# Optimization experiments

Measured on AMD Instinct MI355X. Metric: run time of the kernel, lower is better.

The kernel has to match this reference:

```python
import jax, jax.numpy as jnp
import numpy as np

B_, T_, D_MODEL = 2, 2048, 1024
EXPAND, D_STATE, D_CONV, HEADDIM = 2, 128, 4, 64
D_INNER = EXPAND * D_MODEL            # 2048
NHEADS = D_INNER // HEADDIM           # 32
CONV_DIM = D_INNER + 2 * D_STATE      # 2304 (x, B, C share the depthwise conv)
D_IN_PROJ = 2 * D_INNER + 2 * D_STATE + NHEADS  # z, xBC, dt


def _rmsnorm(x, w, eps=1e-5):
    return x * jax.lax.rsqrt(jnp.mean(x * x, axis=-1, keepdims=True) + eps) * w


def setup_inputs() -> dict:
    key = jax.random.key(0)
    ks = jax.random.split(key, 8)
    def s(k, shape, scale=0.02):
        return jax.random.normal(k, shape, jnp.float32) * scale
    x = jax.random.normal(ks[0], (B_, T_, D_MODEL), jnp.float32)
    W_in = s(ks[1], (D_MODEL, D_IN_PROJ))
    conv_w = s(ks[2], (CONV_DIM, D_CONV), 0.1)
    conv_b = jnp.zeros((CONV_DIM,), jnp.float32)
    # dt_bias = softplus^-1(dt_init) with dt in [1e-3, 1e-1], per Mamba init
    dt0 = jax.random.uniform(ks[3], (NHEADS,), minval=1e-3, maxval=1e-1)
    dt_bias = jnp.log(jnp.expm1(dt0))
    A_log = jnp.log(jax.random.uniform(ks[4], (NHEADS,), minval=1.0, maxval=16.0))
    D = jnp.ones((NHEADS,), jnp.float32)
    norm_w = jnp.ones((D_MODEL,), jnp.float32)
    gnorm_w = jnp.ones((D_INNER,), jnp.float32)
    W_out = s(ks[5], (D_INNER, D_MODEL))
    return {"x": x, "W_in": W_in, "conv_w": conv_w, "conv_b": conv_b,
            "dt_bias": dt_bias, "A_log": A_log, "D": D,
            "norm_w": norm_w, "gnorm_w": gnorm_w, "W_out": W_out}


def reference(x, W_in, conv_w, conv_b, dt_bias, A_log, D, norm_w, gnorm_w, W_out):
    res = x
    xn = _rmsnorm(x, norm_w)                       # pre-norm
    zxbcdt = xn @ W_in                             # (B,T,D_IN_PROJ)
    z = zxbcdt[..., :D_INNER]
    xBC = zxbcdt[..., D_INNER:D_INNER + CONV_DIM]
    dt = zxbcdt[..., D_INNER + CONV_DIM:]          # (B,T,H)
    # causal depthwise conv over time on concat(x,B,C)
    inp = jnp.transpose(xBC, (0, 2, 1))            # (B,C,T)
    kern = conv_w[:, None, :]                      # (C,1,K)
    conv = jax.lax.conv_general_dilated(
        inp, kern, window_strides=(1,), padding=[(D_CONV - 1, 0)],
        feature_group_count=CONV_DIM, dimension_numbers=("NCH", "OIH", "NCH"))
    xBC = jax.nn.silu(jnp.transpose(conv, (0, 2, 1)) + conv_b)
    xs = xBC[..., :D_INNER].reshape(B_, T_, NHEADS, HEADDIM)  # (B,T,H,P)
    Bm = xBC[..., D_INNER:D_INNER + D_STATE]       # (B,T,N), ngroups=1
    C = xBC[..., D_INNER + D_STATE:]               # (B,T,N)
    dt = jax.nn.softplus(dt + dt_bias)             # (B,T,H)
    A = -jnp.exp(A_log)                            # (H,)

    def step(h, inps):
        x_t, B_t, C_t, dt_t = inps                 # (B,H,P),(B,N),(B,N),(B,H)
        da = jnp.exp(dt_t * A)                     # (B,H)
        h = h * da[:, :, None, None] + (dt_t[..., None] * x_t)[..., None] * B_t[:, None, None, :]
        y = jnp.einsum("bhpn,bn->bhp", h, C_t) + D[None, :, None] * x_t
        return h, y

    h0 = jnp.zeros((B_, NHEADS, HEADDIM, D_STATE), x.dtype)
    seq = (jnp.moveaxis(xs, 1, 0), jnp.moveaxis(Bm, 1, 0),
           jnp.moveaxis(C, 1, 0), jnp.moveaxis(dt, 1, 0))
    _, ys = jax.lax.scan(step, h0, seq)            # ys: (T,B,H,P)
    y = jnp.moveaxis(ys, 0, 1).reshape(B_, T_, D_INNER)
    y = _rmsnorm(y * jax.nn.silu(z), gnorm_w)      # gated RMSNorm
    return y @ W_out + res
```

## Files before the change

kernel.cpp:

```cpp
#include <hip/hip_runtime.h>
#include <hip/hip_bf16.h>

typedef unsigned short u16;
typedef unsigned int u32;
typedef u16 u16x8 __attribute__((ext_vector_type(8)));
typedef __bf16 bf16x8 __attribute__((ext_vector_type(8)));
typedef float f32x4 __attribute__((ext_vector_type(4)));

#define B_SZ 2
#define T_SZ 2048
#define DMODEL 1024
#define DINNER 2048
#define DSTATE 128
#define NHEADS 32
#define HEADDIM 64
#define CONVDIM 2304
#define DINPROJ 4384
#define DINPROJ_P 4480
#define NROWS (B_SZ * T_SZ)
#define L_CH 128
#define NCH 16

__device__ __forceinline__ float bf2f(u16 u) {
    union { float f; u32 i; } v; v.i = ((u32)u) << 16; return v.f;
}
__device__ __forceinline__ u16 f2bf(float f) {
    union { float f; u32 i; } v; v.f = f;
    u32 r = v.i + 0x7FFFu + ((v.i >> 16) & 1u);
    return (u16)(r >> 16);
}
__device__ __forceinline__ bf16x8 ldfrag(const u16* p) {
    return __builtin_bit_cast(bf16x8, *(const u16x8*)p);
}
__device__ __forceinline__ void gload_lds16(const u16* g, u16* l) {
    __builtin_amdgcn_global_load_lds(
        (const __attribute__((address_space(1))) unsigned int*)g,
        (__attribute__((address_space(3))) unsigned int*)l, 16, 0, 0);
}

__device__ void trans_tile(const float* __restrict__ in, u16* __restrict__ out,
                           int K, int N, int n0, int k0)
{
    __shared__ u16 tile[64][66];
    const int tid = threadIdx.x;
#pragma unroll
    for (int r = 0; r < 16; r++) {
        int idx = r * 256 + tid;
        int k = idx >> 6, n = idx & 63;
        float v = (n0 + n < N) ? in[(size_t)(k0 + k) * N + n0 + n] : 0.f;
        tile[n][k] = f2bf(v);
    }
    __syncthreads();
#pragma unroll
    for (int r = 0; r < 16; r++) {
        int idx = r * 256 + tid;
        int n = idx >> 6, k = idx & 63;
        out[(size_t)(n0 + n) * K + k0 + k] = tile[n][k];
    }
}

__global__ __launch_bounds__(256) void prep_kernel(
    const float* __restrict__ W_in, u16* __restrict__ W_inT,
    const float* __restrict__ W_out, u16* __restrict__ W_outT,
    const float* __restrict__ x, const float* __restrict__ nw, u16* __restrict__ xn,
    const float* __restrict__ cw, u16* __restrict__ cwT)
{
    const int blk = blockIdx.x;
    const int tid = threadIdx.x;
    if (blk < 1120) {
        trans_tile(W_in, W_inT, DMODEL, DINPROJ, (blk % 70) * 64, (blk / 70) * 64);
    } else if (blk < 1632) {
        int idx = blk - 1120;
        trans_tile(W_out, W_outT, DINNER, DMODEL, (idx % 16) * 64, (idx / 16) * 64);
    } else if (blk < 5728) {
        const int row = blk - 1632;
        const float* xr = x + (size_t)row * DMODEL;
        float vals[4]; float ss = 0.f;
#pragma unroll
        for (int i = 0; i < 4; i++) {
            int c = tid + i * 256;
            float v = xr[c]; vals[i] = v; ss += v * v;
        }
#pragma unroll
        for (int o = 32; o; o >>= 1) ss += __shfl_xor(ss, o);
        __shared__ float red[4];
        if ((tid & 63) == 0) red[tid >> 6] = ss;
        __syncthreads();
        ss = red[0] + red[1] + red[2] + red[3];
        float sc = rsqrtf(ss / (float)DMODEL + 1e-5f);
#pragma unroll
        for (int i = 0; i < 4; i++) {
            int c = tid + i * 256;
            xn[(size_t)row * DMODEL + c] = f2bf(vals[i] * sc * nw[c]);
        }
    } else {
        for (int idx = tid; idx < 4 * CONVDIM; idx += 256) {
            int k = idx / CONVDIM, c = idx - k * CONVDIM;
            cwT[idx] = f2bf(cw[c * 4 + k]);
        }
    }
}

template<int MODE, int KC>
__global__ __launch_bounds__(256) void gemm128_kernel(
    const u16* __restrict__ A, const u16* __restrict__ BT, void* __restrict__ Cv,
    const float* __restrict__ Res, int Nst, int nbx)
{
    __shared__ u16 As[128 * 64];
    __shared__ u16 Bs[128 * 64];
    const int tid = threadIdx.x;
    const int l = tid & 63, w = tid >> 6;
    const int per = nbx * 8;
    const int grp = blockIdx.x / per, r = blockIdx.x % per;
    const int m0 = (grp * 8 + (r & 7)) * 128;
    const int n0 = (r >> 3) * 128;
    const int ml = l & 15, quad = l >> 4;
    const int wm = (w & 1) * 64, wn = (w >> 1) * 64;
    f32x4 acc[4][4] = {};
    const int srow = l >> 3;
    const int sgx = (l & 7) ^ srow;
    const u16* Ag = A + (size_t)(m0 + w * 8 + srow) * KC + sgx * 8;
    const u16* Bg = BT + (size_t)(n0 + w * 8 + srow) * KC + sgx * 8;
    u16* const As_w = &As[(w * 8) * 64];
    u16* const Bs_w = &Bs[(w * 8) * 64];

#pragma unroll 4
    for (int k0 = 0; k0 < KC; k0 += 64) {
        __syncthreads();
#pragma unroll
        for (int j = 0; j < 4; j++) {
            gload_lds16(Ag + (size_t)(j * 32) * KC + k0, As_w + j * 32 * 64);
            gload_lds16(Bg + (size_t)(j * 32) * KC + k0, Bs_w + j * 32 * 64);
        }
        __syncthreads();
#pragma unroll
        for (int ks4 = 0; ks4 < 2; ks4++) {
            bf16x8 af[4], bfr[4];
#pragma unroll
            for (int i = 0; i < 4; i++)
                af[i] = ldfrag(&As[(wm + i * 16 + ml) * 64 +
                                   (((ks4 * 4 + quad) ^ (ml & 7)) * 8)]);
#pragma unroll
            for (int i = 0; i < 4; i++)
                bfr[i] = ldfrag(&Bs[(wn + i * 16 + ml) * 64 +
                                    (((ks4 * 4 + quad) ^ (ml & 7)) * 8)]);
#pragma unroll
            for (int mt = 0; mt < 4; mt++)
#pragma unroll
                for (int nt = 0; nt < 4; nt++)
                    acc[mt][nt] = __builtin_amdgcn_mfma_f32_16x16x32_bf16(
                        af[mt], bfr[nt], acc[mt][nt], 0, 0, 0);
        }
    }
#pragma unroll
    for (int mt = 0; mt < 4; mt++)
#pragma unroll
        for (int nt = 0; nt < 4; nt++)
#pragma unroll
            for (int rg = 0; rg < 4; rg++) {
                int m = m0 + wm + mt * 16 + quad * 4 + rg;
                int n = n0 + wn + nt * 16 + ml;
                if (n < Nst) {
                    if (MODE == 0)
                        ((u16*)Cv)[(size_t)m * Nst + n] = f2bf(acc[mt][nt][rg]);
                    else
                        ((float*)Cv)[(size_t)m * Nst + n] =
                            acc[mt][nt][rg] + Res[(size_t)m * Nst + n];
                }
            }
}

template<int KC>
__global__ __launch_bounds__(256) void gemm128x64_kernel(
    const u16* __restrict__ A, const u16* __restrict__ BT, float* __restrict__ C,
    const float* __restrict__ Res, int Nst)
{
    __shared__ u16 As[128 * 64];
    __shared__ u16 Bs[64 * 64];
    const int tid = threadIdx.x;
    const int l = tid & 63, w = tid >> 6;
    const int m0 = blockIdx.y * 128;
    const int n0 = blockIdx.x * 64;
    const int ml = l & 15, quad = l >> 4;
    const int wm = w * 32;
    f32x4 acc[2][4] = {};
    const int srow = l >> 3;
    const int sgx = (l & 7) ^ srow;
    const u16* Ag = A + (size_t)(m0 + w * 8 + srow) * KC + sgx * 8;
    const u16* Bg = BT + (size_t)(n0 + w * 8 + srow) * KC + sgx * 8;
    u16* const As_w = &As[(w * 8) * 64];
    u16* const Bs_w = &Bs[(w * 8) * 64];

#pragma unroll 4
    for (int k0 = 0; k0 < KC; k0 += 64) {
        __syncthreads();
#pragma unroll
        for (int j = 0; j < 4; j++)
            gload_lds16(Ag + (size_t)(j * 32) * KC + k0, As_w + j * 32 * 64);
#pragma unroll
        for (int j = 0; j < 2; j++)
            gload_lds16(Bg + (size_t)(j * 32) * KC + k0, Bs_w + j * 32 * 64);
        __syncthreads();
#pragma unroll
        for (int ks4 = 0; ks4 < 2; ks4++) {
            bf16x8 af[2], bfr[4];
#pragma unroll
            for (int i = 0; i < 2; i++)
                af[i] = ldfrag(&As[(wm + i * 16 + ml) * 64 +
                                   (((ks4 * 4 + quad) ^ (ml & 7)) * 8)]);
#pragma unroll
            for (int i = 0; i < 4; i++)
                bfr[i] = ldfrag(&Bs[(i * 16 + ml) * 64 +
                                    (((ks4 * 4 + quad) ^ (ml & 7)) * 8)]);
#pragma unroll
            for (int mt = 0; mt < 2; mt++)
#pragma unroll
                for (int nt = 0; nt < 4; nt++)
                    acc[mt][nt] = __builtin_amdgcn_mfma_f32_16x16x32_bf16(
                        af[mt], bfr[nt], acc[mt][nt], 0, 0, 0);
        }
    }
#pragma unroll
    for (int mt = 0; mt < 2; mt++)
#pragma unroll
        for (int nt = 0; nt < 4; nt++)
#pragma unroll
            for (int rg = 0; rg < 4; rg++) {
                int m = m0 + wm + mt * 16 + quad * 4 + rg;
                int n = n0 + nt * 16 + ml;
                C[(size_t)m * Nst + n] = acc[mt][nt][rg] + Res[(size_t)m * Nst + n];
            }
}

#define NGRAN (CONVDIM / 8)
__global__ __launch_bounds__(256) void conv_silu_kernel(
    const u16* __restrict__ zx, const u16* __restrict__ cwT,
    const float* __restrict__ cb, const float* __restrict__ dt_bias,
    u16* __restrict__ out, float* __restrict__ dts)
{
    int idx = blockIdx.x * 256 + threadIdx.x;
    if (idx < B_SZ * NHEADS * T_SZ) {
        int t = idx & (T_SZ - 1);
        int bh = idx >> 11;
        int h = bh & 31, b = bh >> 5;
        float v = bf2f(zx[(size_t)(b * T_SZ + t) * DINPROJ + (DINNER + CONVDIM) + h]) + dt_bias[h];
        float sp = (v > 20.f) ? v : log1pf(expf(v));
        dts[((size_t)bh << 11) + t] = sp;
    }
    int gr = idx % NGRAN;
    int bt = idx / NGRAN;
    int t = bt & (T_SZ - 1);
    int c0 = gr * 8;
    float acc[8];
#pragma unroll
    for (int u = 0; u < 8; u++) acc[u] = cb[c0 + u];
    const u16* base = zx + (size_t)bt * DINPROJ + DINNER + c0;
#pragma unroll
    for (int k = 0; k < 4; k++) {
        int tt = t - 3 + k;
        if (tt >= 0) {
            u16x8 xv = *(const u16x8*)(base + (ptrdiff_t)(k - 3) * DINPROJ);
            u16x8 wv = *(const u16x8*)&cwT[k * CONVDIM + c0];
#pragma unroll
            for (int u = 0; u < 8; u++)
                acc[u] += bf2f(xv[u]) * bf2f(wv[u]);
        }
    }
    u16 res[8];
#pragma unroll
    for (int u = 0; u < 8; u++) {
        float s = acc[u] / (1.f + expf(-acc[u]));
        res[u] = f2bf(s);
    }
    *(u16x8*)&out[(size_t)bt * CONVDIM + c0] = *(u16x8*)res;
}

__global__ __launch_bounds__(256) void chunk_state_kernel(
    const u16* __restrict__ xbc, const float* __restrict__ dts_g,
    const float* __restrict__ A_log, float* __restrict__ cs_g, u16* __restrict__ S_bf)
{
    const int g = blockIdx.x;
    const int b = g >> 9, rem = g & 511, c = rem >> 5, h = rem & 31;
    const int tid = threadIdx.x;
    __shared__ float tmp[128], dt_l[128], d2e[128];
    __shared__ u16 Xw[64][136];
    __shared__ u16 BsT[128][136];
    const float A = -__expf(A_log[h]);
    if (tid < 128) {
        float d = dts_g[(((size_t)(b * 32 + h)) << 11) + (c << 7) + tid];
        dt_l[tid] = d; tmp[tid] = d * A;
    }
    __syncthreads();
    for (int off = 1; off < 128; off <<= 1) {
        float add = 0.f;
        if (tid < 128 && tid >= off) add = tmp[tid - off];
        __syncthreads();
        if (tid < 128) tmp[tid] += add;
        __syncthreads();
    }
    if (tid < 128) {
        float cs = tmp[tid];
        cs_g[(((size_t)(b * 32 + h)) << 11) + (c << 7) + tid] = cs;
        d2e[tid] = __expf(tmp[127] - cs) * dt_l[tid];
    }
    __syncthreads();
    const size_t rowbase = ((size_t)(b * T_SZ + c * L_CH)) * CONVDIM;
#pragma unroll
    for (int r = 0; r < 4; r++) {
        int v = tid + r * 256;
        int t = v >> 3, p0 = (v & 7) << 3;
        u16x8 xv = *(const u16x8*)&xbc[rowbase + (size_t)t * CONVDIM + h * 64 + p0];
        float s = d2e[t];
#pragma unroll
        for (int u = 0; u < 8; u++) Xw[p0 + u][t] = f2bf(bf2f(xv[u]) * s);
    }
#pragma unroll
    for (int r = 0; r < 8; r++) {
        int v = tid + r * 256;
        int t = v >> 4, n0 = (v & 15) << 3;
        u16x8 bv = *(const u16x8*)&xbc[rowbase + (size_t)t * CONVDIM + DINNER + n0];
#pragma unroll
        for (int u = 0; u < 8; u++) BsT[n0 + u][t] = bv[u];
    }
    __syncthreads();
    const int lane = tid & 63, wv = tid >> 6, ml = lane & 15, quad = lane >> 4;
    f32x4 acc[8] = {};
    for (int k0 = 0; k0 < 128; k0 += 32) {
        bf16x8 af = ldfrag(&Xw[wv * 16 + ml][k0 + quad * 8]);
#pragma unroll
        for (int nt = 0; nt < 8; nt++) {
            bf16x8 bf = ldfrag(&BsT[nt * 16 + ml][k0 + quad * 8]);
            acc[nt] = __builtin_amdgcn_mfma_f32_16x16x32_bf16(af, bf, acc[nt], 0, 0, 0);
        }
    }
    const size_t base = (size_t)g * 8192;
#pragma unroll
    for (int nt = 0; nt < 8; nt++) {
#pragma unroll
        for (int rg = 0; rg < 4; rg++) {
            int p = wv * 16 + quad * 4 + rg, n = nt * 16 + ml;
            S_bf[base + p * 128 + n] = f2bf(acc[nt][rg]);
        }
    }
}

__global__ __launch_bounds__(256) void state_pass_kernel(
    const float* __restrict__ cs_g, u16* __restrict__ S_bf)
{
    const int bh = blockIdx.x, b = bh >> 5, h = bh & 31;
    const int tid = threadIdx.x;
    float H[32];
#pragma unroll
    for (int i = 0; i < 32; i++) H[i] = 0.f;
    for (int c = 0; c < NCH; c++) {
        float decay = __expf(cs_g[(((size_t)(b * 32 + h)) << 11) + (c << 7) + 127]);
        size_t slot = ((size_t)((b * NCH + c) * 32 + h)) * 8192 + tid * 32;
        u16 tv[32];
#pragma unroll
        for (int q = 0; q < 4; q++)
            *(u16x8*)&tv[q * 8] = *(const u16x8*)&S_bf[slot + q * 8];
        u16 hw[32];
#pragma unroll
        for (int i = 0; i < 32; i++) hw[i] = f2bf(H[i]);
#pragma unroll
        for (int q = 0; q < 4; q++)
            *(u16x8*)&S_bf[slot + q * 8] = *(const u16x8*)&hw[q * 8];
#pragma unroll
        for (int i = 0; i < 32; i++) H[i] = H[i] * decay + bf2f(tv[i]);
    }
}

__global__ __launch_bounds__(256) void chunk_out_kernel(
    const u16* __restrict__ xbc, const float* __restrict__ dts_g,
    const float* __restrict__ cs_g, const u16* __restrict__ H_bf,
    const float* __restrict__ Dv, u16* __restrict__ yraw)
{
    const int g = blockIdx.x;
    const int b = g >> 9, rem = g & 511, c = rem >> 5, h = rem & 31;
    const int tid = threadIdx.x;
    __shared__ u16 Xs[64][136];
    __shared__ u16 Gs[128][40];
    __shared__ float cs_l[128], P_l[128], dt_l[128];
    const size_t rowbase = ((size_t)(b * T_SZ + c * L_CH)) * CONVDIM;
    const u16* Cg = xbc + rowbase + DINNER + 128;
    const u16* Bg = xbc + rowbase + DINNER;
    const u16* Hg = H_bf + (size_t)g * 8192;
    if (tid < 128) {
        float cs = cs_g[(((size_t)(b * 32 + h)) << 11) + (c << 7) + tid];
        cs_l[tid] = cs; P_l[tid] = __expf(cs);
        dt_l[tid] = dts_g[(((size_t)(b * 32 + h)) << 11) + (c << 7) + tid];
    }
#pragma unroll
    for (int r = 0; r < 4; r++) {
        int v = tid + r * 256; int t = v >> 3, p0 = (v & 7) << 3;
        u16x8 xv = *(const u16x8*)&xbc[rowbase + (size_t)t * CONVDIM + h * 64 + p0];
#pragma unroll
        for (int u = 0; u < 8; u++) Xs[p0 + u][t] = xv[u];
    }
    __syncthreads();
    const int lane = tid & 63, wv = tid >> 6, ml = lane & 15, quad = lane >> 4;
    const int trow = wv * 32;
    f32x4 accY[2][4] = {};
    for (int k0 = 0; k0 < 128; k0 += 32) {
        bf16x8 af0 = ldfrag(Cg + (size_t)(trow + ml) * CONVDIM + k0 + quad * 8);
        bf16x8 af1 = ldfrag(Cg + (size_t)(trow + 16 + ml) * CONVDIM + k0 + quad * 8);
#pragma unroll
        for (int pt = 0; pt < 4; pt++) {
            bf16x8 bf = ldfrag(Hg + (pt * 16 + ml) * 128 + k0 + quad * 8);
            accY[0][pt] = __builtin_amdgcn_mfma_f32_16x16x32_bf16(af0, bf, accY[0][pt], 0, 0, 0);
            accY[1][pt] = __builtin_amdgcn_mfma_f32_16x16x32_bf16(af1, bf, accY[1][pt], 0, 0, 0);
        }
    }
#pragma unroll
    for (int mt = 0; mt < 2; mt++) {
#pragma unroll
        for (int rg = 0; rg < 4; rg++) {
            float pp = P_l[trow + mt * 16 + quad * 4 + rg];
#pragma unroll
            for (int pt = 0; pt < 4; pt++) accY[mt][pt][rg] *= pp;
        }
    }
    for (int js = 0; js < 4; js++) {
        const int j0 = js * 32;
        f32x4 Ga[2][2] = {};
        for (int k0 = 0; k0 < 128; k0 += 32) {
            bf16x8 af0 = ldfrag(Cg + (size_t)(trow + ml) * CONVDIM + k0 + quad * 8);
            bf16x8 af1 = ldfrag(Cg + (size_t)(trow + 16 + ml) * CONVDIM + k0 + quad * 8);
            bf16x8 bf0 = ldfrag(Bg + (size_t)(j0 + ml) * CONVDIM + k0 + quad * 8);
            bf16x8 bf1 = ldfrag(Bg + (size_t)(j0 + 16 + ml) * CONVDIM + k0 + quad * 8);
            Ga[0][0] = __builtin_amdgcn_mfma_f32_16x16x32_bf16(af0, bf0, Ga[0][0], 0, 0, 0);
            Ga[0][1] = __builtin_amdgcn_mfma_f32_16x16x32_bf16(af0, bf1, Ga[0][1], 0, 0, 0);
            Ga[1][0] = __builtin_amdgcn_mfma_f32_16x16x32_bf16(af1, bf0, Ga[1][0], 0, 0, 0);
            Ga[1][1] = __builtin_amdgcn_mfma_f32_16x16x32_bf16(af1, bf1, Ga[1][1], 0, 0, 0);
        }
#pragma unroll
        for (int mt = 0; mt < 2; mt++) {
#pragma unroll
            for (int jt = 0; jt < 2; jt++) {
#pragma unroll
                for (int rg = 0; rg < 4; rg++) {
                    int t = trow + mt * 16 + quad * 4 + rg;
                    int j = j0 + jt * 16 + ml;
                    float val = 0.f;
                    if (t >= j) val = Ga[mt][jt][rg] * __expf(cs_l[t] - cs_l[j]) * dt_l[j];
                    Gs[t][jt * 16 + ml] = f2bf(val);
                }
            }
        }
#pragma unroll
        for (int mt = 0; mt < 2; mt++) {
            bf16x8 af = ldfrag(&Gs[trow + mt * 16 + ml][quad * 8]);
#pragma unroll
            for (int pt = 0; pt < 4; pt++) {
                bf16x8 bf = ldfrag(&Xs[pt * 16 + ml][j0 + quad * 8]);
                accY[mt][pt] = __builtin_amdgcn_mfma_f32_16x16x32_bf16(af, bf, accY[mt][pt], 0, 0, 0);
            }
        }
    }
    const float Dh = Dv[h];
    const size_t ybase = ((size_t)(b * T_SZ + c * L_CH)) * DINNER;
#pragma unroll
    for (int mt = 0; mt < 2; mt++) {
#pragma unroll
        for (int pt = 0; pt < 4; pt++) {
#pragma unroll
            for (int rg = 0; rg < 4; rg++) {
                int t = trow + mt * 16 + quad * 4 + rg;
                int p = pt * 16 + ml;
                float v = accY[mt][pt][rg] + Dh * bf2f(Xs[p][t]);
                yraw[ybase + (size_t)t * DINNER + h * 64 + p] = f2bf(v);
            }
        }
    }
}

__global__ __launch_bounds__(256) void postnorm_kernel(
    const u16* __restrict__ yraw, const u16* __restrict__ zx,
    const float* __restrict__ gw, u16* __restrict__ out)
{
    const int row = blockIdx.x;
    const u16* yr = yraw + (size_t)row * DINNER;
    const u16* zr = zx + (size_t)row * DINPROJ;
    float vals[8]; float ss = 0.f;
#pragma unroll
    for (int i = 0; i < 8; i++) {
        int c = threadIdx.x + i * 256;
        float y = bf2f(yr[c]);
        float z = bf2f(zr[c]);
        float s = z / (1.f + expf(-z));
        float t = y * s; vals[i] = t; ss += t * t;
    }
#pragma unroll
    for (int o = 32; o; o >>= 1) ss += __shfl_xor(ss, o);
    __shared__ float red[4];
    if ((threadIdx.x & 63) == 0) red[threadIdx.x >> 6] = ss;
    __syncthreads();
    ss = red[0] + red[1] + red[2] + red[3];
    float sc = rsqrtf(ss / (float)DINNER + 1e-5f);
#pragma unroll
    for (int i = 0; i < 8; i++) {
        int c = threadIdx.x + i * 256;
        out[(size_t)row * DINNER + c] = f2bf(vals[i] * sc * gw[c]);
    }
}

extern "C" void kernel_launch(void* const* d_in, const int* in_sizes, int n_in,
                              void* d_out, int out_size, void* d_ws, size_t ws_size,
                              hipStream_t stream) {
    const float* x       = (const float*)d_in[0];
    const float* W_in    = (const float*)d_in[1];
    const float* conv_w  = (const float*)d_in[2];
    const float* conv_b  = (const float*)d_in[3];
    const float* dt_bias = (const float*)d_in[4];
    const float* A_log   = (const float*)d_in[5];
    const float* Dv      = (const float*)d_in[6];
    const float* norm_w  = (const float*)d_in[7];
    const float* gnorm_w = (const float*)d_in[8];
    const float* W_out   = (const float*)d_in[9];
    float* out = (float*)d_out;

    char* ws = (char*)d_ws;
    u16*   xn    = (u16*)(ws);
    u16*   W_inT = (u16*)(ws + 8388608);
    u16*   S_bf  = (u16*)(ws);
    float* cs_g  = (float*)(ws + 16777216);
    u16*   zx    = (u16*)(ws + 17563648);
    u16*   xbc   = (u16*)(ws + 53477376);
    float* dts   = (float*)(ws + 72351744);
    u16*   yraw  = (u16*)(ws + 72876032);
    u16*   cwT   = (u16*)(ws + 89653248);
    u16*   W_outT= (u16*)(ws + 89671680);
    u16*   ynorm = yraw;

    prep_kernel<<<5729, 256, 0, stream>>>(
        W_in, W_inT, W_out, W_outT, x, norm_w, xn, conv_w, cwT);
    gemm128_kernel<0, DMODEL><<<(DINPROJ_P / 128) * (NROWS / 128), 256, 0, stream>>>(
        xn, W_inT, zx, nullptr, DINPROJ, DINPROJ_P / 128);
    conv_silu_kernel<<<(NROWS * NGRAN) / 256, 256, 0, stream>>>(
        zx, cwT, conv_b, dt_bias, xbc, dts);
    chunk_state_kernel<<<B_SZ * NCH * NHEADS, 256, 0, stream>>>(xbc, dts, A_log, cs_g, S_bf);
    state_pass_kernel<<<B_SZ * NHEADS, 256, 0, stream>>>(cs_g, S_bf);
    chunk_out_kernel<<<B_SZ * NCH * NHEADS, 256, 0, stream>>>(xbc, dts, cs_g, S_bf, Dv, yraw);
    postnorm_kernel<<<NROWS, 256, 0, stream>>>(yraw, zx, gnorm_w, ynorm);
    gemm128x64_kernel<DINNER><<<dim3(DMODEL / 64, NROWS / 128), 256, 0, stream>>>(
        ynorm, W_outT, out, x, DMODEL);
}
```

Measured before the change: 299.1 us.

## Pipeline in-projection GEMM with 256x256 tiles and vectorize memory-bound kernels

Replaces the 128x128 in-projection GEMM with a 512-thread 256x256-tile kernel. It double-buffers LDS, interleaves global-to-LDS staging with MFMA sub-steps, and raises wave priority during the matrix ops. The leftover columns are handled by a separate 128x64 GEMM launch. It also vectorizes the weight transpose, RMSNorm prep and postnorm loads/stores, and spreads the state-pass across 8x more blocks with 4 elements per thread. The larger tile trades a smaller grid (256 blocks) and heavier register/LDS use for better data reuse.

```diff
diff --git a/kernel.cpp b/kernel.cpp
--- a/kernel.cpp
+++ b/kernel.cpp
@@ -4,6 +4,7 @@
 typedef unsigned short u16;
 typedef unsigned int u32;
 typedef u16 u16x8 __attribute__((ext_vector_type(8)));
+typedef u16 u16x4 __attribute__((ext_vector_type(4)));
 typedef __bf16 bf16x8 __attribute__((ext_vector_type(8)));
 typedef float f32x4 __attribute__((ext_vector_type(4)));
 
@@ -41,21 +42,34 @@
 __device__ void trans_tile(const float* __restrict__ in, u16* __restrict__ out,
                            int K, int N, int n0, int k0)
 {
-    __shared__ u16 tile[64][66];
+    __shared__ u16 tile[64][72];
     const int tid = threadIdx.x;
 #pragma unroll
-    for (int r = 0; r < 16; r++) {
+    for (int r = 0; r < 4; r++) {
         int idx = r * 256 + tid;
-        int k = idx >> 6, n = idx & 63;
-        float v = (n0 + n < N) ? in[(size_t)(k0 + k) * N + n0 + n] : 0.f;
-        tile[n][k] = f2bf(v);
+        int k = idx >> 4, n4 = (idx & 15) << 2;
+        const float* src = &in[(size_t)(k0 + k) * N + n0 + n4];
+        float4 v;
+        if (n0 + n4 + 3 < N) {
+            v = *(const float4*)src;
+        } else {
+            v.x = (n0 + n4 + 0 < N) ? src[0] : 0.f;
+            v.y = (n0 + n4 + 1 < N) ? src[1] : 0.f;
+            v.z = (n0 + n4 + 2 < N) ? src[2] : 0.f;
+            v.w = (n0 + n4 + 3 < N) ? src[3] : 0.f;
+        }
+        tile[n4 + 0][k] = f2bf(v.x);
+        tile[n4 + 1][k] = f2bf(v.y);
+        tile[n4 + 2][k] = f2bf(v.z);
+        tile[n4 + 3][k] = f2bf(v.w);
     }
     __syncthreads();
 #pragma unroll
-    for (int r = 0; r < 16; r++) {
+    for (int r = 0; r < 2; r++) {
         int idx = r * 256 + tid;
-        int n = idx >> 6, k = idx & 63;
-        out[(size_t)(n0 + n) * K + k0 + k] = tile[n][k];
+        int n = idx >> 3, k8 = (idx & 7) << 3;
+        u16x8 vv = *(const u16x8*)&tile[n][k8];
+        *(u16x8*)&out[(size_t)(n0 + n) * K + k0 + k8] = vv;
     }
 }
 
@@ -74,13 +88,8 @@
         trans_tile(W_out, W_outT, DINNER, DMODEL, (idx % 16) * 64, (idx / 16) * 64);
     } else if (blk < 5728) {
         const int row = blk - 1632;
-        const float* xr = x + (size_t)row * DMODEL;
-        float vals[4]; float ss = 0.f;
-#pragma unroll
-        for (int i = 0; i < 4; i++) {
-            int c = tid + i * 256;
-            float v = xr[c]; vals[i] = v; ss += v * v;
-        }
+        float4 v = ((const float4*)(x + (size_t)row * DMODEL))[tid];
+        float ss = v.x * v.x + v.y * v.y + v.z * v.z + v.w * v.w;
 #pragma unroll
         for (int o = 32; o; o >>= 1) ss += __shfl_xor(ss, o);
         __shared__ float red[4];
@@ -88,11 +97,13 @@
         __syncthreads();
         ss = red[0] + red[1] + red[2] + red[3];
         float sc = rsqrtf(ss / (float)DMODEL + 1e-5f);
-#pragma unroll
-        for (int i = 0; i < 4; i++) {
-            int c = tid + i * 256;
-            xn[(size_t)row * DMODEL + c] = f2bf(vals[i] * sc * nw[c]);
-        }
+        float4 wv = ((const float4*)nw)[tid];
+        u16x4 o4;
+        o4[0] = f2bf(v.x * sc * wv.x);
+        o4[1] = f2bf(v.y * sc * wv.y);
+        o4[2] = f2bf(v.z * sc * wv.z);
+        o4[3] = f2bf(v.w * sc * wv.w);
+        *(u16x4*)&xn[(size_t)row * DMODEL + tid * 4] = o4;
     } else {
         for (int idx = tid; idx < 4 * CONVDIM; idx += 256) {
             int k = idx / CONVDIM, c = idx - k * CONVDIM;
@@ -101,79 +112,122 @@
     }
 }
 
-template<int MODE, int KC>
-__global__ __launch_bounds__(256) void gemm128_kernel(
-    const u16* __restrict__ A, const u16* __restrict__ BT, void* __restrict__ Cv,
-    const float* __restrict__ Res, int Nst, int nbx)
-{
-    __shared__ u16 As[128 * 64];
-    __shared__ u16 Bs[128 * 64];
+template<int KC>
+__global__ __launch_bounds__(512, 2) void gemm256_kernel(
+    const u16* __restrict__ A, const u16* __restrict__ BT, u16* __restrict__ C,
+    int Nst, int Brows, int nbn)
+{
+    __shared__ u16 As[2 * 256 * 64];
+    __shared__ u16 Bs[2 * 256 * 64];
     const int tid = threadIdx.x;
     const int l = tid & 63, w = tid >> 6;
-    const int per = nbx * 8;
-    const int grp = blockIdx.x / per, r = blockIdx.x % per;
-    const int m0 = (grp * 8 + (r & 7)) * 128;
-    const int n0 = (r >> 3) * 128;
+    const int wm = w >> 2, wn = w & 3;
     const int ml = l & 15, quad = l >> 4;
-    const int wm = (w & 1) * 64, wn = (w >> 1) * 64;
-    f32x4 acc[4][4] = {};
-    const int srow = l >> 3;
-    const int sgx = (l & 7) ^ srow;
-    const u16* Ag = A + (size_t)(m0 + w * 8 + srow) * KC + sgx * 8;
-    const u16* Bg = BT + (size_t)(n0 + w * 8 + srow) * KC + sgx * 8;
-    u16* const As_w = &As[(w * 8) * 64];
-    u16* const Bs_w = &Bs[(w * 8) * 64];
-
-#pragma unroll 4
-    for (int k0 = 0; k0 < KC; k0 += 64) {
-        __syncthreads();
-#pragma unroll
-        for (int j = 0; j < 4; j++) {
-            gload_lds16(Ag + (size_t)(j * 32) * KC + k0, As_w + j * 32 * 64);
-            gload_lds16(Bg + (size_t)(j * 32) * KC + k0, Bs_w + j * 32 * 64);
-        }
-        __syncthreads();
-#pragma unroll
-        for (int ks4 = 0; ks4 < 2; ks4++) {
-            bf16x8 af[4], bfr[4];
-#pragma unroll
-            for (int i = 0; i < 4; i++)
-                af[i] = ldfrag(&As[(wm + i * 16 + ml) * 64 +
-                                   (((ks4 * 4 + quad) ^ (ml & 7)) * 8)]);
-#pragma unroll
-            for (int i = 0; i < 4; i++)
-                bfr[i] = ldfrag(&Bs[(wn + i * 16 + ml) * 64 +
-                                    (((ks4 * 4 + quad) ^ (ml & 7)) * 8)]);
-#pragma unroll
-            for (int mt = 0; mt < 4; mt++)
-#pragma unroll
-                for (int nt = 0; nt < 4; nt++)
-                    acc[mt][nt] = __builtin_amdgcn_mfma_f32_16x16x32_bf16(
-                        af[mt], bfr[nt], acc[mt][nt], 0, 0, 0);
-        }
-    }
-#pragma unroll
-    for (int mt = 0; mt < 4; mt++)
+    const int srow = l >> 3, sgx = (l & 7) ^ srow;
+
+    const int bid = blockIdx.x;
+    const int wg = (bid & 7) * (gridDim.x >> 3) + (bid >> 3);
+    const int m0 = (wg / nbn) * 256;
+    const int n0 = (wg % nbn) * 256;
+    const int bcap = Brows - 1 - n0;
+
+    const u16* Ag = A + (size_t)m0 * KC;
+    const u16* Bg = BT + (size_t)n0 * KC;
+    const int NT = KC / 64;
+
+    f32x4 acc[8][4] = {};
+    bf16x8 af[4][2];
+    bf16x8 bfr[2][2][2];
+
+#define BARX() { asm volatile("" ::: "memory"); __builtin_amdgcn_s_barrier(); asm volatile("" ::: "memory"); }
+#define STG(Gp, Lp, bsel, hs, kt, cap)                                        \
+    { const int kcol_ = (kt) * 64;                                            \
+      _Pragma("unroll")                                                       \
+      for (int j_ = 0; j_ < 2; j_++) {                                        \
+          const int i0_ = (w * 2 + j_) * 8;                                   \
+          const int r0_ = (i0_ & 63) + ((i0_ >> 6) << 7) + ((hs) << 6);       \
+          int gr_ = r0_ + srow; if (gr_ > (cap)) gr_ = (cap);                 \
+          gload_lds16(Gp + (size_t)gr_ * KC + kcol_ + sgx * 8,                \
+                      Lp + (bsel) * 16384 + r0_ * 64);                        \
+      } }
+#define RDA(bsel, qm)                                                         \
+    _Pragma("unroll") for (int mt_ = 0; mt_ < 4; mt_++)                       \
+    _Pragma("unroll") for (int ks_ = 0; ks_ < 2; ks_++)                       \
+        af[mt_][ks_] = ldfrag(&As[(bsel) * 16384 +                            \
+            (wm * 128 + ((qm) * 4 + mt_) * 16 + ml) * 64 +                    \
+            (((ks_ * 4 + quad) ^ (ml & 7)) * 8)]);
+#define RDB(bsel, qn)                                                         \
+    _Pragma("unroll") for (int nt_ = 0; nt_ < 2; nt_++)                       \
+    _Pragma("unroll") for (int ks_ = 0; ks_ < 2; ks_++)                       \
+        bfr[qn][nt_][ks_] = ldfrag(&Bs[(bsel) * 16384 +                       \
+            (wn * 64 + ((qn) * 2 + nt_) * 16 + ml) * 64 +                     \
+            (((ks_ * 4 + quad) ^ (ml & 7)) * 8)]);
+#define MMA(qm, qn)                                                           \
+    __builtin_amdgcn_s_setprio(1);                                            \
+    _Pragma("unroll") for (int ks_ = 0; ks_ < 2; ks_++)                       \
+    _Pragma("unroll") for (int mt_ = 0; mt_ < 4; mt_++)                       \
+    _Pragma("unroll") for (int nt_ = 0; nt_ < 2; nt_++)                       \
+        acc[(qm) * 4 + mt_][(qn) * 2 + nt_] =                                 \
+            __builtin_amdgcn_mfma_f32_16x16x32_bf16(                          \
+                af[mt_][ks_], bfr[qn][nt_][ks_],                              \
+                acc[(qm) * 4 + mt_][(qn) * 2 + nt_], 0, 0, 0);                \
+    __builtin_amdgcn_s_setprio(0);
+
+    STG(Ag, As, 0, 0, 0, 255);
+    STG(Bg, Bs, 0, 0, 0, bcap);
+    STG(Bg, Bs, 0, 1, 0, bcap);
+    STG(Ag, As, 0, 1, 0, bcap < 255 ? bcap : 255);
+    STG(Ag, As, 1, 0, 1, 255);
+    STG(Bg, Bs, 1, 0, 1, bcap);
+    asm volatile("s_waitcnt vmcnt(4)" ::: "memory");
+    BARX();
+
+#define TILE(t, bsel)                                                         \
+    { const bool s1_ = (t) + 1 < NT, s2_ = (t) + 2 < NT;                      \
+      RDA(bsel, 0); RDB(bsel, 0);                                             \
+      if (s1_) STG(Bg, Bs, (bsel) ^ 1, 1, (t) + 1, bcap);                     \
+      BARX(); MMA(0, 0); BARX();                                              \
+      RDB(bsel, 1);                                                           \
+      if (s1_) STG(Ag, As, (bsel) ^ 1, 1, (t) + 1, 255);                      \
+      BARX(); MMA(0, 1); BARX();                                              \
+      RDA(bsel, 1);                                                           \
+      if (s2_) STG(Ag, As, bsel, 0, (t) + 2, 255);                            \
+      BARX(); MMA(1, 0); BARX();                                              \
+      if (s2_) { STG(Bg, Bs, bsel, 0, (t) + 2, bcap);                         \
+                 asm volatile("s_waitcnt vmcnt(4)" ::: "memory"); }           \
+      else     { asm volatile("s_waitcnt vmcnt(0)" ::: "memory"); }           \
+      BARX(); MMA(1, 1); BARX(); }
+
+#pragma unroll 1
+    for (int t = 0; t < NT; t += 2) {
+        TILE(t, 0);
+        TILE(t + 1, 1);
+    }
+#undef TILE
+#undef MMA
+#undef RDB
+#undef RDA
+#undef STG
+#undef BARX
+
+#pragma unroll
+    for (int mt = 0; mt < 8; mt++)
 #pragma unroll
         for (int nt = 0; nt < 4; nt++)
 #pragma unroll
             for (int rg = 0; rg < 4; rg++) {
-                int m = m0 + wm + mt * 16 + quad * 4 + rg;
-                int n = n0 + wn + nt * 16 + ml;
-                if (n < Nst) {
-                    if (MODE == 0)
-                        ((u16*)Cv)[(size_t)m * Nst + n] = f2bf(acc[mt][nt][rg]);
-                    else
-                        ((float*)Cv)[(size_t)m * Nst + n] =
-                            acc[mt][nt][rg] + Res[(size_t)m * Nst + n];
-                }
+                int m = m0 + wm * 128 + mt * 16 + quad * 4 + rg;
+                int n = n0 + wn * 64 + nt * 16 + ml;
+                if (n < Nst)
+                    C[(size_t)m * Nst + n] = f2bf(acc[mt][nt][rg]);
             }
 }
 
-template<int KC>
+
+template<int KC, int MODE>
 __global__ __launch_bounds__(256) void gemm128x64_kernel(
-    const u16* __restrict__ A, const u16* __restrict__ BT, float* __restrict__ C,
-    const float* __restrict__ Res, int Nst)
+    const u16* __restrict__ A, const u16* __restrict__ BT, void* __restrict__ Cv,
+    const float* __restrict__ Res, int Nst, int Nlim)
 {
     __shared__ u16 As[128 * 64];
     __shared__ u16 Bs[64 * 64];
@@ -228,7 +282,13 @@
             for (int rg = 0; rg < 4; rg++) {
                 int m = m0 + wm + mt * 16 + quad * 4 + rg;
                 int n = n0 + nt * 16 + ml;
-                C[(size_t)m * Nst + n] = acc[mt][nt][rg] + Res[(size_t)m * Nst + n];
+                if (n < Nlim) {
+                    if (MODE == 0)
+                        ((u16*)Cv)[(size_t)m * Nst + n] = f2bf(acc[mt][nt][rg]);
+                    else
+                        ((float*)Cv)[(size_t)m * Nst + n] =
+                            acc[mt][nt][rg] + Res[(size_t)m * Nst + n];
+                }
             }
 }
 
@@ -347,26 +407,20 @@
 __global__ __launch_bounds__(256) void state_pass_kernel(
     const float* __restrict__ cs_g, u16* __restrict__ S_bf)
 {
-    const int bh = blockIdx.x, b = bh >> 5, h = bh & 31;
-    const int tid = threadIdx.x;
-    float H[32];
-#pragma unroll
-    for (int i = 0; i < 32; i++) H[i] = 0.f;
+    const int bh = blockIdx.x >> 3, b = bh >> 5, h = bh & 31;
+    const int off = (blockIdx.x & 7) * 1024 + threadIdx.x * 4;
+    const float* csb = cs_g + (((size_t)(b * 32 + h)) << 11);
+    float H[4] = {0.f, 0.f, 0.f, 0.f};
     for (int c = 0; c < NCH; c++) {
-        float decay = __expf(cs_g[(((size_t)(b * 32 + h)) << 11) + (c << 7) + 127]);
-        size_t slot = ((size_t)((b * NCH + c) * 32 + h)) * 8192 + tid * 32;
-        u16 tv[32];
-#pragma unroll
-        for (int q = 0; q < 4; q++)
-            *(u16x8*)&tv[q * 8] = *(const u16x8*)&S_bf[slot + q * 8];
-        u16 hw[32];
-#pragma unroll
-        for (int i = 0; i < 32; i++) hw[i] = f2bf(H[i]);
-#pragma unroll
-        for (int q = 0; q < 4; q++)
-            *(u16x8*)&S_bf[slot + q * 8] = *(const u16x8*)&hw[q * 8];
-#pragma unroll
-        for (int i = 0; i < 32; i++) H[i] = H[i] * decay + bf2f(tv[i]);
+        float decay = __expf(csb[(c << 7) + 127]);
+        size_t slot = ((size_t)((b * NCH + c) * 32 + h)) * 8192 + off;
+        u16x4 tv = *(const u16x4*)&S_bf[slot];
+        u16x4 hw;
+#pragma unroll
+        for (int i = 0; i < 4; i++) hw[i] = f2bf(H[i]);
+        *(u16x4*)&S_bf[slot] = hw;
+#pragma unroll
+        for (int i = 0; i < 4; i++) H[i] = H[i] * decay + bf2f(tv[i]);
     }
 }
 
@@ -479,29 +533,28 @@
     const float* __restrict__ gw, u16* __restrict__ out)
 {
     const int row = blockIdx.x;
-    const u16* yr = yraw + (size_t)row * DINNER;
-    const u16* zr = zx + (size_t)row * DINPROJ;
+    const int tid = threadIdx.x;
+    u16x8 yv = *(const u16x8*)(yraw + (size_t)row * DINNER + tid * 8);
+    u16x8 zv = *(const u16x8*)(zx + (size_t)row * DINPROJ + tid * 8);
     float vals[8]; float ss = 0.f;
 #pragma unroll
     for (int i = 0; i < 8; i++) {
-        int c = threadIdx.x + i * 256;
-        float y = bf2f(yr[c]);
-        float z = bf2f(zr[c]);
+        float y = bf2f(yv[i]);
+        float z = bf2f(zv[i]);
         float s = z / (1.f + expf(-z));
         float t = y * s; vals[i] = t; ss += t * t;
     }
 #pragma unroll
     for (int o = 32; o; o >>= 1) ss += __shfl_xor(ss, o);
     __shared__ float red[4];
-    if ((threadIdx.x & 63) == 0) red[threadIdx.x >> 6] = ss;
+    if ((tid & 63) == 0) red[tid >> 6] = ss;
     __syncthreads();
     ss = red[0] + red[1] + red[2] + red[3];
     float sc = rsqrtf(ss / (float)DINNER + 1e-5f);
-#pragma unroll
-    for (int i = 0; i < 8; i++) {
-        int c = threadIdx.x + i * 256;
-        out[(size_t)row * DINNER + c] = f2bf(vals[i] * sc * gw[c]);
-    }
+    u16 o8[8];
+#pragma unroll
+    for (int i = 0; i < 8; i++) o8[i] = f2bf(vals[i] * sc * gw[tid * 8 + i]);
+    *(u16x8*)(out + (size_t)row * DINNER + tid * 8) = *(u16x8*)o8;
 }
 
 extern "C" void kernel_launch(void* const* d_in, const int* in_sizes, int n_in,
@@ -534,14 +587,17 @@
 
     prep_kernel<<<5729, 256, 0, stream>>>(
         W_in, W_inT, W_out, W_outT, x, norm_w, xn, conv_w, cwT);
-    gemm128_kernel<0, DMODEL><<<(DINPROJ_P / 128) * (NROWS / 128), 256, 0, stream>>>(
-        xn, W_inT, zx, nullptr, DINPROJ, DINPROJ_P / 128);
+    gemm256_kernel<DMODEL><<<256, 512, 0, stream>>>(
+        xn, W_inT, zx, DINPROJ, DINPROJ_P, 16);
+    gemm128x64_kernel<DMODEL, 0><<<dim3(5, NROWS / 128), 256, 0, stream>>>(
+        xn, W_inT + (size_t)4096 * DMODEL, zx + 4096, nullptr,
+        DINPROJ, DINPROJ - 4096);
     conv_silu_kernel<<<(NROWS * NGRAN) / 256, 256, 0, stream>>>(
         zx, cwT, conv_b, dt_bias, xbc, dts);
     chunk_state_kernel<<<B_SZ * NCH * NHEADS, 256, 0, stream>>>(xbc, dts, A_log, cs_g, S_bf);
-    state_pass_kernel<<<B_SZ * NHEADS, 256, 0, stream>>>(cs_g, S_bf);
+    state_pass_kernel<<<B_SZ * NHEADS * 8, 256, 0, stream>>>(cs_g, S_bf);
     chunk_out_kernel<<<B_SZ * NCH * NHEADS, 256, 0, stream>>>(xbc, dts, cs_g, S_bf, Dv, yraw);
     postnorm_kernel<<<NROWS, 256, 0, stream>>>(yraw, zx, gnorm_w, ynorm);
-    gemm128x64_kernel<DINNER><<<dim3(DMODEL / 64, NROWS / 128), 256, 0, stream>>>(
-        ynorm, W_outT, out, x, DMODEL);
-}
+    gemm128x64_kernel<DINNER, 1><<<dim3(DMODEL / 64, NROWS / 128), 256, 0, stream>>>(
+        ynorm, W_outT, out, x, DMODEL, DMODEL);
+}
```

Measured after the change: 285.5 us. 1.05x faster.

## Vectorize memory accesses across kernels and widen state pass parallelism

Applied to the files above, without the earlier changes.

Vectorizes global loads and stores in the weight transpose, input RMSNorm, GEMM epilogue, chunk-state store and postnorm kernels, swapping MFMA operand order so each lane holds contiguous output columns. The state pass is split into 8x more blocks, each handling a 1024-element slice with prefetch of the next chunk. Chunk_out hoists C and B fragments into registers and reuses them across loops. This cuts uncoalesced scalar memory traffic and raises occupancy of the serial state pass, at the cost of more registers.

```diff
diff --git a/kernel.cpp b/kernel.cpp
--- a/kernel.cpp
+++ b/kernel.cpp
@@ -4,6 +4,7 @@
 typedef unsigned short u16;
 typedef unsigned int u32;
 typedef u16 u16x8 __attribute__((ext_vector_type(8)));
+typedef u16 u16x4 __attribute__((ext_vector_type(4)));
 typedef __bf16 bf16x8 __attribute__((ext_vector_type(8)));
 typedef float f32x4 __attribute__((ext_vector_type(4)));
 
@@ -41,21 +42,34 @@
 __device__ void trans_tile(const float* __restrict__ in, u16* __restrict__ out,
                            int K, int N, int n0, int k0)
 {
-    __shared__ u16 tile[64][66];
-    const int tid = threadIdx.x;
-#pragma unroll
-    for (int r = 0; r < 16; r++) {
+    __shared__ u16 tile[64][72];
+    const int tid = threadIdx.x;
+#pragma unroll
+    for (int r = 0; r < 4; r++) {
         int idx = r * 256 + tid;
-        int k = idx >> 6, n = idx & 63;
-        float v = (n0 + n < N) ? in[(size_t)(k0 + k) * N + n0 + n] : 0.f;
-        tile[n][k] = f2bf(v);
+        int k = idx >> 4, n4 = (idx & 15) << 2;
+        const float* src = &in[(size_t)(k0 + k) * N + n0 + n4];
+        float4 v;
+        if (n0 + n4 + 3 < N) {
+            v = *(const float4*)src;
+        } else {
+            v.x = (n0 + n4 + 0 < N) ? src[0] : 0.f;
+            v.y = (n0 + n4 + 1 < N) ? src[1] : 0.f;
+            v.z = (n0 + n4 + 2 < N) ? src[2] : 0.f;
+            v.w = (n0 + n4 + 3 < N) ? src[3] : 0.f;
+        }
+        tile[n4 + 0][k] = f2bf(v.x);
+        tile[n4 + 1][k] = f2bf(v.y);
+        tile[n4 + 2][k] = f2bf(v.z);
+        tile[n4 + 3][k] = f2bf(v.w);
     }
     __syncthreads();
 #pragma unroll
-    for (int r = 0; r < 16; r++) {
+    for (int r = 0; r < 2; r++) {
         int idx = r * 256 + tid;
-        int n = idx >> 6, k = idx & 63;
-        out[(size_t)(n0 + n) * K + k0 + k] = tile[n][k];
+        int n = idx >> 3, k8 = (idx & 7) << 3;
+        u16x8 vv = *(const u16x8*)&tile[n][k8];
+        *(u16x8*)&out[(size_t)(n0 + n) * K + k0 + k8] = vv;
     }
 }
 
@@ -74,13 +88,8 @@
         trans_tile(W_out, W_outT, DINNER, DMODEL, (idx % 16) * 64, (idx / 16) * 64);
     } else if (blk < 5728) {
         const int row = blk - 1632;
-        const float* xr = x + (size_t)row * DMODEL;
-        float vals[4]; float ss = 0.f;
-#pragma unroll
-        for (int i = 0; i < 4; i++) {
-            int c = tid + i * 256;
-            float v = xr[c]; vals[i] = v; ss += v * v;
-        }
+        float4 v = ((const float4*)(x + (size_t)row * DMODEL))[tid];
+        float ss = v.x * v.x + v.y * v.y + v.z * v.z + v.w * v.w;
 #pragma unroll
         for (int o = 32; o; o >>= 1) ss += __shfl_xor(ss, o);
         __shared__ float red[4];
@@ -88,11 +97,13 @@
         __syncthreads();
         ss = red[0] + red[1] + red[2] + red[3];
         float sc = rsqrtf(ss / (float)DMODEL + 1e-5f);
-#pragma unroll
-        for (int i = 0; i < 4; i++) {
-            int c = tid + i * 256;
-            xn[(size_t)row * DMODEL + c] = f2bf(vals[i] * sc * nw[c]);
-        }
+        float4 wv = ((const float4*)nw)[tid];
+        u16x4 o4;
+        o4[0] = f2bf(v.x * sc * wv.x);
+        o4[1] = f2bf(v.y * sc * wv.y);
+        o4[2] = f2bf(v.z * sc * wv.z);
+        o4[3] = f2bf(v.w * sc * wv.w);
+        *(u16x4*)&xn[(size_t)row * DMODEL + tid * 4] = o4;
     } else {
         for (int idx = tid; idx < 4 * CONVDIM; idx += 256) {
             int k = idx / CONVDIM, c = idx - k * CONVDIM;
@@ -217,19 +228,24 @@
 #pragma unroll
                 for (int nt = 0; nt < 4; nt++)
                     acc[mt][nt] = __builtin_amdgcn_mfma_f32_16x16x32_bf16(
-                        af[mt], bfr[nt], acc[mt][nt], 0, 0, 0);
-        }
-    }
-#pragma unroll
-    for (int mt = 0; mt < 2; mt++)
-#pragma unroll
-        for (int nt = 0; nt < 4; nt++)
-#pragma unroll
-            for (int rg = 0; rg < 4; rg++) {
-                int m = m0 + wm + mt * 16 + quad * 4 + rg;
-                int n = n0 + nt * 16 + ml;
-                C[(size_t)m * Nst + n] = acc[mt][nt][rg] + Res[(size_t)m * Nst + n];
-            }
+                        bfr[nt], af[mt], acc[mt][nt], 0, 0, 0);
+        }
+    }
+#pragma unroll
+    for (int mt = 0; mt < 2; mt++) {
+        const int m = m0 + wm + mt * 16 + ml;
+#pragma unroll
+        for (int nt = 0; nt < 4; nt++) {
+            const int nb = n0 + nt * 16 + quad * 4;
+            float4 r = *(const float4*)&Res[(size_t)m * Nst + nb];
+            float4 o;
+            o.x = acc[mt][nt][0] + r.x;
+            o.y = acc[mt][nt][1] + r.y;
+            o.z = acc[mt][nt][2] + r.z;
+            o.w = acc[mt][nt][3] + r.w;
+            *(float4*)&C[(size_t)m * Nst + nb] = o;
+        }
+    }
 }
 
 #define NGRAN (CONVDIM / 8)
@@ -330,43 +346,42 @@
 #pragma unroll
         for (int nt = 0; nt < 8; nt++) {
             bf16x8 bf = ldfrag(&BsT[nt * 16 + ml][k0 + quad * 8]);
-            acc[nt] = __builtin_amdgcn_mfma_f32_16x16x32_bf16(af, bf, acc[nt], 0, 0, 0);
+            acc[nt] = __builtin_amdgcn_mfma_f32_16x16x32_bf16(bf, af, acc[nt], 0, 0, 0);
         }
     }
     const size_t base = (size_t)g * 8192;
+    const int p = wv * 16 + ml;
 #pragma unroll
     for (int nt = 0; nt < 8; nt++) {
-#pragma unroll
-        for (int rg = 0; rg < 4; rg++) {
-            int p = wv * 16 + quad * 4 + rg, n = nt * 16 + ml;
-            S_bf[base + p * 128 + n] = f2bf(acc[nt][rg]);
-        }
+        const int nb = nt * 16 + quad * 4;
+        u16x4 pk;
+#pragma unroll
+        for (int rg = 0; rg < 4; rg++) pk[rg] = f2bf(acc[nt][rg]);
+        *(u16x4*)&S_bf[base + p * 128 + nb] = pk;
     }
 }
 
 __global__ __launch_bounds__(256) void state_pass_kernel(
     const float* __restrict__ cs_g, u16* __restrict__ S_bf)
 {
-    const int bh = blockIdx.x, b = bh >> 5, h = bh & 31;
-    const int tid = threadIdx.x;
-    float H[32];
-#pragma unroll
-    for (int i = 0; i < 32; i++) H[i] = 0.f;
+    const int bh = blockIdx.x >> 3, b = bh >> 5, h = bh & 31;
+    const int off = (blockIdx.x & 7) * 1024 + threadIdx.x * 4;
+    const float* csb = cs_g + (((size_t)(b * 32 + h)) << 11);
+    float H[4] = {0.f, 0.f, 0.f, 0.f};
+    const size_t step = (size_t)32 * 8192;
+    size_t slot = ((size_t)(b * NCH * 32 + h)) * 8192 + off;
+    u16x4 tv = *(const u16x4*)&S_bf[slot];
     for (int c = 0; c < NCH; c++) {
-        float decay = __expf(cs_g[(((size_t)(b * 32 + h)) << 11) + (c << 7) + 127]);
-        size_t slot = ((size_t)((b * NCH + c) * 32 + h)) * 8192 + tid * 32;
-        u16 tv[32];
-#pragma unroll
-        for (int q = 0; q < 4; q++)
-            *(u16x8*)&tv[q * 8] = *(const u16x8*)&S_bf[slot + q * 8];
-        u16 hw[32];
-#pragma unroll
-        for (int i = 0; i < 32; i++) hw[i] = f2bf(H[i]);
-#pragma unroll
-        for (int q = 0; q < 4; q++)
-            *(u16x8*)&S_bf[slot + q * 8] = *(const u16x8*)&hw[q * 8];
-#pragma unroll
-        for (int i = 0; i < 32; i++) H[i] = H[i] * decay + bf2f(tv[i]);
+        u16x4 tvn = tv;
+        if (c + 1 < NCH) tvn = *(const u16x4*)&S_bf[slot + step];
+        float decay = __expf(csb[(c << 7) + 127]);
+        u16x4 hw;
+#pragma unroll
+        for (int i = 0; i < 4; i++) hw[i] = f2bf(H[i]);
+        *(u16x4*)&S_bf[slot] = hw;
+#pragma unroll
+        for (int i = 0; i < 4; i++) H[i] = H[i] * decay + bf2f(tv[i]);
+        tv = tvn; slot += step;
     }
 }
 
@@ -400,15 +415,20 @@
     __syncthreads();
     const int lane = tid & 63, wv = tid >> 6, ml = lane & 15, quad = lane >> 4;
     const int trow = wv * 32;
+    bf16x8 cf[2][4];
+#pragma unroll
+    for (int mt = 0; mt < 2; mt++)
+#pragma unroll
+        for (int kk = 0; kk < 4; kk++)
+            cf[mt][kk] = ldfrag(Cg + (size_t)(trow + mt * 16 + ml) * CONVDIM + kk * 32 + quad * 8);
     f32x4 accY[2][4] = {};
-    for (int k0 = 0; k0 < 128; k0 += 32) {
-        bf16x8 af0 = ldfrag(Cg + (size_t)(trow + ml) * CONVDIM + k0 + quad * 8);
-        bf16x8 af1 = ldfrag(Cg + (size_t)(trow + 16 + ml) * CONVDIM + k0 + quad * 8);
+#pragma unroll
+    for (int kk = 0; kk < 4; kk++) {
 #pragma unroll
         for (int pt = 0; pt < 4; pt++) {
-            bf16x8 bf = ldfrag(Hg + (pt * 16 + ml) * 128 + k0 + quad * 8);
-            accY[0][pt] = __builtin_amdgcn_mfma_f32_16x16x32_bf16(af0, bf, accY[0][pt], 0, 0, 0);
-            accY[1][pt] = __builtin_amdgcn_mfma_f32_16x16x32_bf16(af1, bf, accY[1][pt], 0, 0, 0);
+            bf16x8 bf = ldfrag(Hg + (pt * 16 + ml) * 128 + kk * 32 + quad * 8);
+            accY[0][pt] = __builtin_amdgcn_mfma_f32_16x16x32_bf16(cf[0][kk], bf, accY[0][pt], 0, 0, 0);
+            accY[1][pt] = __builtin_amdgcn_mfma_f32_16x16x32_bf16(cf[1][kk], bf, accY[1][pt], 0, 0, 0);
         }
     }
 #pragma unroll
@@ -419,19 +439,29 @@
 #pragma unroll
             for (int pt = 0; pt < 4; pt++) accY[mt][pt][rg] *= pp;
         }
+    }
+    bf16x8 bp[4][2];
+#pragma unroll
+    for (int kk = 0; kk < 4; kk++) {
+        bp[kk][0] = ldfrag(Bg + (size_t)(ml) * CONVDIM + kk * 32 + quad * 8);
+        bp[kk][1] = ldfrag(Bg + (size_t)(16 + ml) * CONVDIM + kk * 32 + quad * 8);
     }
     for (int js = 0; js < 4; js++) {
         const int j0 = js * 32;
         f32x4 Ga[2][2] = {};
-        for (int k0 = 0; k0 < 128; k0 += 32) {
-            bf16x8 af0 = ldfrag(Cg + (size_t)(trow + ml) * CONVDIM + k0 + quad * 8);
-            bf16x8 af1 = ldfrag(Cg + (size_t)(trow + 16 + ml) * CONVDIM + k0 + quad * 8);
-            bf16x8 bf0 = ldfrag(Bg + (size_t)(j0 + ml) * CONVDIM + k0 + quad * 8);
-            bf16x8 bf1 = ldfrag(Bg + (size_t)(j0 + 16 + ml) * CONVDIM + k0 + quad * 8);
-            Ga[0][0] = __builtin_amdgcn_mfma_f32_16x16x32_bf16(af0, bf0, Ga[0][0], 0, 0, 0);
-            Ga[0][1] = __builtin_amdgcn_mfma_f32_16x16x32_bf16(af0, bf1, Ga[0][1], 0, 0, 0);
-            Ga[1][0] = __builtin_amdgcn_mfma_f32_16x16x32_bf16(af1, bf0, Ga[1][0], 0, 0, 0);
-            Ga[1][1] = __builtin_amdgcn_mfma_f32_16x16x32_bf16(af1, bf1, Ga[1][1], 0, 0, 0);
+#pragma unroll
+        for (int kk = 0; kk < 4; kk++) {
+            Ga[0][0] = __builtin_amdgcn_mfma_f32_16x16x32_bf16(cf[0][kk], bp[kk][0], Ga[0][0], 0, 0, 0);
+            Ga[0][1] = __builtin_amdgcn_mfma_f32_16x16x32_bf16(cf[0][kk], bp[kk][1], Ga[0][1], 0, 0, 0);
+            Ga[1][0] = __builtin_amdgcn_mfma_f32_16x16x32_bf16(cf[1][kk], bp[kk][0], Ga[1][0], 0, 0, 0);
+            Ga[1][1] = __builtin_amdgcn_mfma_f32_16x16x32_bf16(cf[1][kk], bp[kk][1], Ga[1][1], 0, 0, 0);
+        }
+        if (js < 3) {
+#pragma unroll
+            for (int kk = 0; kk < 4; kk++) {
+                bp[kk][0] = ldfrag(Bg + (size_t)(j0 + 32 + ml) * CONVDIM + kk * 32 + quad * 8);
+                bp[kk][1] = ldfrag(Bg + (size_t)(j0 + 48 + ml) * CONVDIM + kk * 32 + quad * 8);
+            }
         }
 #pragma unroll
         for (int mt = 0; mt < 2; mt++) {
@@ -449,11 +479,11 @@
         }
 #pragma unroll
         for (int mt = 0; mt < 2; mt++) {
-            bf16x8 af = ldfrag(&Gs[trow + mt * 16 + ml][quad * 8]);
+            bf16x8 ag = ldfrag(&Gs[trow + mt * 16 + ml][quad * 8]);
 #pragma unroll
             for (int pt = 0; pt < 4; pt++) {
-                bf16x8 bf = ldfrag(&Xs[pt * 16 + ml][j0 + quad * 8]);
-                accY[mt][pt] = __builtin_amdgcn_mfma_f32_16x16x32_bf16(af, bf, accY[mt][pt], 0, 0, 0);
+                bf16x8 bx = ldfrag(&Xs[pt * 16 + ml][j0 + quad * 8]);
+                accY[mt][pt] = __builtin_amdgcn_mfma_f32_16x16x32_bf16(ag, bx, accY[mt][pt], 0, 0, 0);
             }
         }
     }
@@ -479,29 +509,28 @@
     const float* __restrict__ gw, u16* __restrict__ out)
 {
     const int row = blockIdx.x;
-    const u16* yr = yraw + (size_t)row * DINNER;
-    const u16* zr = zx + (size_t)row * DINPROJ;
+    const int tid = threadIdx.x;
+    u16x8 yv = *(const u16x8*)(yraw + (size_t)row * DINNER + tid * 8);
+    u16x8 zv = *(const u16x8*)(zx + (size_t)row * DINPROJ + tid * 8);
     float vals[8]; float ss = 0.f;
 #pragma unroll
     for (int i = 0; i < 8; i++) {
-        int c = threadIdx.x + i * 256;
-        float y = bf2f(yr[c]);
-        float z = bf2f(zr[c]);
+        float y = bf2f(yv[i]);
+        float z = bf2f(zv[i]);
         float s = z / (1.f + expf(-z));
         float t = y * s; vals[i] = t; ss += t * t;
     }
 #pragma unroll
     for (int o = 32; o; o >>= 1) ss += __shfl_xor(ss, o);
     __shared__ float red[4];
-    if ((threadIdx.x & 63) == 0) red[threadIdx.x >> 6] = ss;
+    if ((tid & 63) == 0) red[tid >> 6] = ss;
     __syncthreads();
     ss = red[0] + red[1] + red[2] + red[3];
     float sc = rsqrtf(ss / (float)DINNER + 1e-5f);
-#pragma unroll
-    for (int i = 0; i < 8; i++) {
-        int c = threadIdx.x + i * 256;
-        out[(size_t)row * DINNER + c] = f2bf(vals[i] * sc * gw[c]);
-    }
+    u16 o8[8];
+#pragma unroll
+    for (int i = 0; i < 8; i++) o8[i] = f2bf(vals[i] * sc * gw[tid * 8 + i]);
+    *(u16x8*)(out + (size_t)row * DINNER + tid * 8) = *(u16x8*)o8;
 }
 
 extern "C" void kernel_launch(void* const* d_in, const int* in_sizes, int n_in,
@@ -539,7 +568,7 @@
     conv_silu_kernel<<<(NROWS * NGRAN) / 256, 256, 0, stream>>>(
         zx, cwT, conv_b, dt_bias, xbc, dts);
     chunk_state_kernel<<<B_SZ * NCH * NHEADS, 256, 0, stream>>>(xbc, dts, A_log, cs_g, S_bf);
-    state_pass_kernel<<<B_SZ * NHEADS, 256, 0, stream>>>(cs_g, S_bf);
+    state_pass_kernel<<<B_SZ * NHEADS * 8, 256, 0, stream>>>(cs_g, S_bf);
     chunk_out_kernel<<<B_SZ * NCH * NHEADS, 256, 0, stream>>>(xbc, dts, cs_g, S_bf, Dv, yraw);
     postnorm_kernel<<<NROWS, 256, 0, stream>>>(yraw, zx, gnorm_w, ynorm);
     gemm128x64_kernel<DINNER><<<dim3(DMODEL / 64, NROWS / 128), 256, 0, stream>>>(
```

After: 281.6 us. 5.8% less time.
